# Optimization experiments

Hardware: AMD Instinct MI355X
Metric: run time of the kernel (lower is better)

The kernel has to match this reference:

```python
import jax, jax.numpy as jnp
import numpy as np

PENETRATION_W = 10.0
STABILITY_W = 1.0
ENERGY_W = 0.1
MIN_DIST = 0.05

B, T, N, D = 16, 100, 128, 3

def setup_inputs() -> dict:
    key = jax.random.key(0)
    k1, k2, k3 = jax.random.split(key, 3)
    trajectories = jax.random.normal(k1, (B, T, N, D), dtype=jnp.float32)
    velocities = jax.random.normal(k2, (B, T, N, D), dtype=jnp.float32)
    forces = jax.random.normal(k3, (B, T, N, D), dtype=jnp.float32)
    return {"trajectories": trajectories, "velocities": velocities, "forces": forces}

def _penetration_loss(trajectories):
    b, t, n, _ = trajectories.shape
    pos = trajectories[..., :3]                                   # [B,T,N,3]
    diff = pos[:, :, :, None, :] - pos[:, :, None, :, :]          # [B,T,N,N,3]
    d2 = jnp.sum(diff * diff, axis=-1)                            # [B,T,N,N]
    mask = jnp.triu(jnp.ones((n, n), dtype=bool), k=1)            # strictly i<j
    # avoid sqrt(0) on diagonal for safe gradients; masked out below
    dist = jnp.sqrt(jnp.where(mask, d2, 1.0))
    pen = jax.nn.relu(MIN_DIST - dist) * mask                     # [B,T,N,N]
    # original: sum over (t, i<j) of mean over batch
    total = jnp.mean(jnp.sum(pen, axis=(1, 2, 3)))
    return total / (t * n * (n - 1) / 2)

def _stability_loss(velocities):
    return jnp.mean(jnp.linalg.norm(velocities[:, -5:], axis=-1))

def _energy_loss(positions, velocities, forces):
    kinetic_start = 0.5 * jnp.mean(jnp.sum(velocities[:, 0] ** 2, axis=-1))
    kinetic_end = 0.5 * jnp.mean(jnp.sum(velocities[:, -1] ** 2, axis=-1))
    displacements = positions[:, 1:] - positions[:, :-1]
    work = jnp.mean(jnp.sum(forces[:, :-1] * displacements, axis=-1))
    return jnp.abs(kinetic_end - kinetic_start - work)

def reference(trajectories, velocities, forces):
    loss = PENETRATION_W * _penetration_loss(trajectories)
    loss = loss + STABILITY_W * _stability_loss(velocities)
    loss = loss + ENERGY_W * _energy_loss(trajectories, velocities, forces)
    return loss
```

## Files before the change

kernel.cpp:

```cpp
#include <hip/hip_runtime.h>
#include <math.h>

constexpr int B = 16, T = 100, N = 128;
constexpr float MIN_DIST  = 0.05f;
constexpr float MIN_DIST2 = MIN_DIST * MIN_DIST;

constexpr int THREADS      = 256;
constexpr int PEN_BLOCKS   = B * T;
constexpr int MISC_BLOCKS  = 160;
constexpr int TOTAL_BLOCKS = PEN_BLOCKS + MISC_BLOCKS;

constexpr int PER_B = T * N * 3;
constexpr int PER_T = N * 3;

constexpr int WORK_V4_PER_B = (T - 1) * N * 3 / 4;
constexpr int WORK_V4 = B * WORK_V4_PER_B;
constexpr int KE_V4_PER_SLICE = N * 3 / 4;
constexpr int KE_V4  = 2 * B * KE_V4_PER_SLICE;
constexpr int STAB_V = B * 5 * N;
constexpr int MISC_TOTAL = WORK_V4 + STAB_V + KE_V4;

constexpr int WORK_N = B * (T - 1) * N;

constexpr int WORK_OFF = 1600, STAB_OFF = 1760, KE0_OFF = 1920, KE1_OFF = 2080;

__device__ __forceinline__ float wave_sum(float v) {
#pragma unroll
    for (int off = 32; off > 0; off >>= 1) v += __shfl_down(v, off, 64);
    return v;
}

__global__ __launch_bounds__(THREADS) void physics_fused(
    const float* __restrict__ traj, const float* __restrict__ vel,
    const float* __restrict__ frc, float* __restrict__ ws)
{
    __shared__ float4 spos[N];
    __shared__ float  red[4][4];

    const int tid  = threadIdx.x;
    const int bid  = blockIdx.x;
    const int lane = tid & 63;
    const int wv   = tid >> 6;

    if (bid < PEN_BLOCKS) {
        const float* p = traj + (size_t)bid * PER_T;
        for (int k = tid; k < N; k += THREADS)
            spos[k] = make_float4(p[k * 3], p[k * 3 + 1], p[k * 3 + 2], 0.f);
        __syncthreads();

        const float4 pa = spos[lane];
        const float4 pb = spos[lane + 64];
        const int jbase = wv * 32;
        float s = 0.f;
#pragma unroll 8
        for (int jj = 0; jj < 32; ++jj) {
            const int j = jbase + jj;
            const float4 pj = spos[j];
            float dx = pa.x - pj.x, dy = pa.y - pj.y, dz = pa.z - pj.z;
            float d2 = dx * dx + dy * dy + dz * dz;
            if (d2 < MIN_DIST2 && j != lane)          s += MIN_DIST - sqrtf(d2);
            dx = pb.x - pj.x; dy = pb.y - pj.y; dz = pb.z - pj.z;
            d2 = dx * dx + dy * dy + dz * dz;
            if (d2 < MIN_DIST2 && j != lane + 64)     s += MIN_DIST - sqrtf(d2);
        }
        float w = wave_sum(s);
        if (lane == 0) red[0][wv] = w;
        __syncthreads();
        if (tid == 0)
            ws[bid] = 0.5f * (red[0][0] + red[0][1] + red[0][2] + red[0][3]);
    } else {
        const int mb = bid - PEN_BLOCKS;
        const float4* t4 = (const float4*)traj;
        const float4* f4 = (const float4*)frc;
        const float4* v4 = (const float4*)vel;
        float sw = 0.f, ss = 0.f, k0 = 0.f, k1 = 0.f;
        const int stride = MISC_BLOCKS * THREADS;
        for (int v = mb * THREADS + tid; v < MISC_TOTAL; v += stride) {
            if (v < WORK_V4) {
                const int b = v / WORK_V4_PER_B;
                const int r = v - b * WORK_V4_PER_B;
                const int base = b * (PER_B / 4) + r;
                const float4 f  = f4[base];
                const float4 t0 = t4[base];
                const float4 t1 = t4[base + PER_T / 4];
                sw += f.x * (t1.x - t0.x) + f.y * (t1.y - t0.y)
                    + f.z * (t1.z - t0.z) + f.w * (t1.w - t0.w);
            } else if (v < WORK_V4 + STAB_V) {
                const int s2 = v - WORK_V4;
                const int b  = s2 / 640;
                const int r  = s2 - b * 640;
                const int e  = b * PER_B + 95 * PER_T + r * 3;
                const float vx = vel[e], vy = vel[e + 1], vz = vel[e + 2];
                ss += sqrtf(vx * vx + vy * vy + vz * vz);
            } else {
                const int s2    = v - WORK_V4 - STAB_V;
                const int which = s2 / 1536;
                const int rr    = s2 - which * 1536;
                const int b     = rr / KE_V4_PER_SLICE;
                const int r     = rr - b * KE_V4_PER_SLICE;
                const float4 q  = v4[b * (PER_B / 4) + which * (99 * PER_T / 4) + r];
                const float k   = q.x * q.x + q.y * q.y + q.z * q.z + q.w * q.w;
                if (which) k1 += k; else k0 += k;
            }
        }
        float vals[4] = {sw, ss, k0, k1};
#pragma unroll
        for (int vv = 0; vv < 4; ++vv) {
            float w = wave_sum(vals[vv]);
            if (lane == 0) red[vv][wv] = w;
        }
        __syncthreads();
        if (tid == 0) {
            ws[WORK_OFF + mb] = red[0][0] + red[0][1] + red[0][2] + red[0][3];
            ws[STAB_OFF + mb] = red[1][0] + red[1][1] + red[1][2] + red[1][3];
            ws[KE0_OFF  + mb] = red[2][0] + red[2][1] + red[2][2] + red[2][3];
            ws[KE1_OFF  + mb] = red[3][0] + red[3][1] + red[3][2] + red[3][3];
        }
    }
}

__global__ __launch_bounds__(256) void physics_finalize(
    const float* __restrict__ ws, float* __restrict__ out)
{
    __shared__ float redP[4], redM[4];
    const int tid = threadIdx.x, lane = tid & 63, wv = tid >> 6;

    float p = 0.f;
    for (int i = tid; i < PEN_BLOCKS; i += 256) p += ws[i];

    const int base = WORK_OFF + 160 * wv;
    float m = ws[base + lane] + ws[base + 64 + lane]
            + (lane < 32 ? ws[base + 128 + lane] : 0.f);

    p = wave_sum(p);
    m = wave_sum(m);
    if (lane == 0) { redP[wv] = p; redM[wv] = m; }
    __syncthreads();

    if (tid == 0) {
        const float pen = redP[0] + redP[1] + redP[2] + redP[3];
        const float wk = redM[0], st = redM[1], k0 = redM[2], k1 = redM[3];
        const float pen_loss  = pen / (float)((long long)B * T * (N * (N - 1) / 2));
        const float stab_loss = st / (float)STAB_V;
        const float ke_s = 0.5f * k0 / (float)(B * N);
        const float ke_e = 0.5f * k1 / (float)(B * N);
        const float work = wk / (float)WORK_N;
        out[0] = 10.0f * pen_loss + stab_loss + 0.1f * fabsf(ke_e - ke_s - work);
    }
}

extern "C" void kernel_launch(void* const* d_in, const int* in_sizes, int n_in,
                              void* d_out, int out_size, void* d_ws, size_t ws_size,
                              hipStream_t stream) {
    const float* traj = (const float*)d_in[0];
    const float* vel  = (const float*)d_in[1];
    const float* frc  = (const float*)d_in[2];
    float* out = (float*)d_out;
    float* ws  = (float*)d_ws;

    physics_fused<<<TOTAL_BLOCKS, THREADS, 0, stream>>>(traj, vel, frc, ws);
    physics_finalize<<<1, 256, 0, stream>>>(ws, out);
}
```

Before: 82.68 us.

## Compute only unique pairs via circular offsets and vectorize position staging

```diff
diff --git a/kernel.cpp b/kernel.cpp
--- a/kernel.cpp
+++ b/kernel.cpp
@@ -35,6 +35,7 @@
     const float* __restrict__ frc, float* __restrict__ ws)
 {
     __shared__ float4 spos[N];
+    __shared__ float  sraw[PER_T];
     __shared__ float  red[4][4];
 
     const int tid  = threadIdx.x;
@@ -42,34 +43,46 @@
     const int lane = tid & 63;
     const int wv   = tid >> 6;
 
-    if (bid < PEN_BLOCKS) {
-        const float* p = traj + (size_t)bid * PER_T;
-        for (int k = tid; k < N; k += THREADS)
-            spos[k] = make_float4(p[k * 3], p[k * 3 + 1], p[k * 3 + 2], 0.f);
+    if (bid >= MISC_BLOCKS) {
+        const int pb = bid - MISC_BLOCKS;
+        if (tid < PER_T / 4)
+            ((float4*)sraw)[tid] = ((const float4*)traj)[pb * (PER_T / 4) + tid];
+        __syncthreads();
+        if (tid < N)
+            spos[tid] = make_float4(sraw[tid * 3], sraw[tid * 3 + 1], sraw[tid * 3 + 2], 0.f);
         __syncthreads();
 
-        const float4 pa = spos[lane];
-        const float4 pb = spos[lane + 64];
-        const int jbase = wv * 32;
+        const int i    = tid & (N - 1);
+        const int half = tid >> 7;
+        const float4 pi = spos[i];
         float s = 0.f;
+        const int k0 = 1 + half * 32;
+        const int k1 = 32 + half * 31;
 #pragma unroll 8
-        for (int jj = 0; jj < 32; ++jj) {
-            const int j = jbase + jj;
+        for (int k = k0; k <= k1; ++k) {
+            const int j = (i + k) & (N - 1);
             const float4 pj = spos[j];
-            float dx = pa.x - pj.x, dy = pa.y - pj.y, dz = pa.z - pj.z;
-            float d2 = dx * dx + dy * dy + dz * dz;
-            if (d2 < MIN_DIST2 && j != lane)          s += MIN_DIST - sqrtf(d2);
-            dx = pb.x - pj.x; dy = pb.y - pj.y; dz = pb.z - pj.z;
-            d2 = dx * dx + dy * dy + dz * dz;
-            if (d2 < MIN_DIST2 && j != lane + 64)     s += MIN_DIST - sqrtf(d2);
+            const float dx = pi.x - pj.x, dy = pi.y - pj.y, dz = pi.z - pj.z;
+            const float d2 = dx * dx + dy * dy + dz * dz;
+            const bool h = d2 < MIN_DIST2;
+            if (__builtin_expect(__any(h), 0))
+                if (h) s += MIN_DIST - sqrtf(d2);
+        }
+        if (half) {
+            const float4 pj = spos[(i + 64) & (N - 1)];
+            const float dx = pi.x - pj.x, dy = pi.y - pj.y, dz = pi.z - pj.z;
+            const float d2 = dx * dx + dy * dy + dz * dz;
+            const bool h = (d2 < MIN_DIST2) & (i < 64);
+            if (__builtin_expect(__any(h), 0))
+                if (h) s += MIN_DIST - sqrtf(d2);
         }
         float w = wave_sum(s);
         if (lane == 0) red[0][wv] = w;
         __syncthreads();
         if (tid == 0)
-            ws[bid] = 0.5f * (red[0][0] + red[0][1] + red[0][2] + red[0][3]);
+            ws[pb] = red[0][0] + red[0][1] + red[0][2] + red[0][3];
     } else {
-        const int mb = bid - PEN_BLOCKS;
+        const int mb = bid;
         const float4* t4 = (const float4*)traj;
         const float4* f4 = (const float4*)frc;
         const float4* v4 = (const float4*)vel;
```

Result: faster. 67.42 us (-18.5%).
